# Performance work log

Measured on AMD Instinct MI355X. Metric: run time of the kernel, lower is better.

The kernel has to match this reference:

```python
import jax, jax.numpy as jnp
import numpy as np

HIDDEN = 1024
HEADS = 16
HEAD_DIM = HIDDEN // HEADS
LN_EPS = 1e-12


def _layer_norm(x, gamma, beta, eps=LN_EPS):
    mu = jnp.mean(x, axis=-1, keepdims=True)
    var = jnp.var(x, axis=-1, keepdims=True)
    return (x - mu) * jax.lax.rsqrt(var + eps) * gamma + beta


def setup_inputs() -> dict:
    key = jax.random.key(0)
    ks = jax.random.split(key, 8)
    B, S = 4, 2048
    hidden_states = jax.random.normal(ks[0], (B, S, HIDDEN), dtype=jnp.float32)
    attention_mask = jnp.zeros((B, 1, 1, S), dtype=jnp.float32)
    scale = 1.0 / np.sqrt(HIDDEN)
    return {
        "hidden_states": hidden_states,
        "attention_mask": attention_mask,
        "ln_gamma": jnp.ones((HIDDEN,), jnp.float32),
        "ln_beta": jnp.zeros((HIDDEN,), jnp.float32),
        "W_qkv": jax.random.normal(ks[1], (HIDDEN, 3 * HIDDEN), jnp.float32) * scale,
        "b_qkv": jnp.zeros((3 * HIDDEN,), jnp.float32),
        "W_out": jax.random.normal(ks[2], (HIDDEN, HIDDEN), jnp.float32) * scale,
        "b_out": jnp.zeros((HIDDEN,), jnp.float32),
    }


def reference(hidden_states, attention_mask, ln_gamma, ln_beta, W_qkv, b_qkv, W_out, b_out):
    B, S, H = hidden_states.shape
    x = _layer_norm(hidden_states, ln_gamma, ln_beta)
    qkv = x @ W_qkv + b_qkv  # [B, S, 3H]
    q, k, v = jnp.split(qkv, 3, axis=-1)
    q = q.reshape(B, S, HEADS, HEAD_DIM)
    k = k.reshape(B, S, HEADS, HEAD_DIM)
    v = v.reshape(B, S, HEADS, HEAD_DIM)
    # scores: [B, heads, q_len, kv_len]
    scores = jnp.einsum("bqhd,bkhd->bhqk", q, k) * (1.0 / np.sqrt(HEAD_DIM))
    scores = scores + attention_mask
    probs = jax.nn.softmax(scores, axis=-1)
    attn = jnp.einsum("bhqk,bkhd->bqhd", probs, v).reshape(B, S, H)
    out = attn @ W_out + b_out
    out = out + hidden_states  # residual (dropout is identity at p=0)
    return out
```

## Files before the change

kernel.cpp:

```cpp
#include <hip/hip_runtime.h>

#define SEQ 2048
#define HID 1024
#define NHEAD 16
#define HDIM 64
#define NB 4
#define NTOK (NB * SEQ)
#define NQKV (3 * HID)
#define LOG2E 1.44269504088896f
#define QSCALE (0.125f * LOG2E)

typedef __attribute__((ext_vector_type(8))) short bf16x8;
typedef __attribute__((ext_vector_type(4))) float f32x4;


__device__ __forceinline__ void glds16(const void* g, void* l) {
  __builtin_amdgcn_global_load_lds(
      (const __attribute__((address_space(1))) void*)g,
      (__attribute__((address_space(3))) void*)l, 16, 0, 0);
}

__device__ __forceinline__ ushort f2bf(float f) {
  union { float f; unsigned int u; } a; a.f = f;
  unsigned int u = a.u;
  return (ushort)((u + 0x7fffu + ((u >> 16) & 1u)) >> 16);
}

__device__ __forceinline__ unsigned int cvtpk(float a, float b) {
  unsigned int r;
  asm("v_cvt_pk_bf16_f32 %0, %1, %2" : "=v"(r) : "v"(a), "v"(b));
  return r;
}


__global__ __launch_bounds__(256) void ln_tr_fused(const float* __restrict__ x,
                                                   const float* __restrict__ g,
                                                   const float* __restrict__ be,
                                                   ushort* __restrict__ y,
                                                   const float* __restrict__ W0,
                                                   ushort* __restrict__ T0,
                                                   const float* __restrict__ W1,
                                                   ushort* __restrict__ T1) {
  __shared__ float t[32][33];
  const int tid = threadIdx.x;
  if (blockIdx.x < NTOK) {
    const int row = blockIdx.x;
    const float4 v = ((const float4*)(x + (size_t)row * HID))[tid];
    float s  = v.x + v.y + v.z + v.w;
    float sq = v.x * v.x + v.y * v.y + v.z * v.z + v.w * v.w;
    for (int o = 1; o < 64; o <<= 1) { s += __shfl_xor(s, o, 64); sq += __shfl_xor(sq, o, 64); }
    const int wv = tid >> 6;
    if ((tid & 63) == 0) { t[0][wv] = s; t[1][wv] = sq; }
    __syncthreads();
    s  = t[0][0] + t[0][1] + t[0][2] + t[0][3];
    sq = t[1][0] + t[1][1] + t[1][2] + t[1][3];
    const float mu  = s * (1.0f / HID);
    const float var = sq * (1.0f / HID) - mu * mu;
    const float rs  = rsqrtf(var + 1e-12f);
    const float4 gv = ((const float4*)g)[tid];
    const float4 bv = ((const float4*)be)[tid];
    ushort4 o;
    o.x = f2bf((v.x - mu) * rs * gv.x + bv.x);
    o.y = f2bf((v.y - mu) * rs * gv.y + bv.y);
    o.z = f2bf((v.z - mu) * rs * gv.z + bv.z);
    o.w = f2bf((v.w - mu) * rs * gv.w + bv.w);
    ((ushort4*)(y + (size_t)row * HID))[tid] = o;
    return;
  }
  const int bid = blockIdx.x - NTOK;
  const float* W; ushort* WT; int C, bx, by;
  if (bid < 3072) { W = W0; WT = T0; C = NQKV; bx = bid % 96; by = bid / 96; }
  else { const int b2 = bid - 3072; W = W1; WT = T1; C = HID; bx = b2 & 31; by = b2 >> 5; }
  const int R = HID;
  const int c0 = bx * 32, r0 = by * 32;
  const int tx = tid & 31, ty = tid >> 5;
  for (int j = 0; j < 4; ++j)
    t[ty + j * 8][tx] = W[(size_t)(r0 + ty + j * 8) * C + c0 + tx];
  __syncthreads();
  for (int j = 0; j < 4; ++j)
    WT[(size_t)(c0 + ty + j * 8) * R + r0 + tx] = f2bf(t[tx][ty + j * 8]);
}


__global__ __launch_bounds__(256) void v_transpose(const ushort* __restrict__ qkv,
                                                   ushort* __restrict__ vt) {
  __shared__ ushort t[64][66];
  const int s0 = blockIdx.x * 64, h = blockIdx.y, b = blockIdx.z;
  const size_t tokbase = (size_t)b * SEQ;
  for (int e = 0; e < 2; ++e) {
    const int c = e * 256 + threadIdx.x;
    const int sr = c >> 3, dc = c & 7;
    *(uint4*)&t[sr][dc * 8] =
        *(const uint4*)(qkv + (tokbase + s0 + sr) * NQKV + 2 * HID + h * HDIM + dc * 8);
  }
  __syncthreads();
  for (int e = 0; e < 2; ++e) {
    const int c = e * 256 + threadIdx.x;
    const int dr = c >> 3, sc = c & 7;
    ushort tmp[8];
    for (int j = 0; j < 8; ++j) tmp[j] = t[sc * 8 + j][dr];
    *(uint4*)(vt + ((size_t)(b * NHEAD + h) * HDIM + dr) * SEQ + s0 + sc * 8) = *(uint4*)tmp;
  }
}


template <int MODE>
__global__ __launch_bounds__(256) void gemm_bt(const ushort* __restrict__ A,
                                               const ushort* __restrict__ Bt,
                                               const float* __restrict__ bias,
                                               const float* __restrict__ resid,
                                               ushort* __restrict__ obf,
                                               float* __restrict__ of32,
                                               ushort* __restrict__ vtob,
                                               int M, int N, int K) {
  __shared__ ushort As[128 * 64];
  __shared__ ushort Bs[128 * 64];
  const int tid = threadIdx.x;
  const int lane = tid & 63, wv = tid >> 6;
  const int q = lane >> 4, li = lane & 15;
  const int nwgx = gridDim.x;
  const int hw = blockIdx.x + nwgx * blockIdx.y;
  const int cpx = (nwgx * gridDim.y) >> 3;
  const int logical = (hw & 7) * cpx + (hw >> 3);
  const int bx = logical % nwgx, by = logical / nwgx;
  const int m0 = by * 128, n0 = bx * 128;
  const int wm = (wv >> 1) * 64, wn = (wv & 1) * 64;
  f32x4 acc[4][4] = {};

  for (int kb = 0; kb < K; kb += 64) {
    for (int e = 0; e < 4; ++e) {
      const int chunk = (wv * 4 + e) * 64 + lane;
      const int row = chunk >> 3, slot = chunk & 7;
      const int kc = slot ^ (row & 7);
      glds16(A  + (size_t)(m0 + row) * K + kb + kc * 8, As + (wv * 4 + e) * 512);
      glds16(Bt + (size_t)(n0 + row) * K + kb + kc * 8, Bs + (wv * 4 + e) * 512);
    }
    __syncthreads();
    for (int ks = 0; ks < 2; ++ks) {
      const int kc = ks * 4 + q;
      bf16x8 af[4], bfr[4];
      for (int mi = 0; mi < 4; ++mi) {
        const int row = wm + mi * 16 + li;
        af[mi] = *(const bf16x8*)(As + (row * 8 + (kc ^ (row & 7))) * 8);
      }
      for (int ni = 0; ni < 4; ++ni) {
        const int row = wn + ni * 16 + li;
        bfr[ni] = *(const bf16x8*)(Bs + (row * 8 + (kc ^ (row & 7))) * 8);
      }
      for (int mi = 0; mi < 4; ++mi)
        for (int ni = 0; ni < 4; ++ni)
          acc[mi][ni] = __builtin_amdgcn_mfma_f32_16x16x32_bf16(af[mi], bfr[ni], acc[mi][ni], 0, 0, 0);
    }
    __syncthreads();
  }

  if (MODE == 0 && vtob != nullptr && n0 >= 2 * HID) {
    const int b = (m0 + wm) >> 11;
    const int sbase = (m0 + wm) & (SEQ - 1);
    for (int ni = 0; ni < 4; ++ni) {
      const int colv = n0 - 2 * HID + wn + ni * 16 + li;
      const int h = colv >> 6, d = colv & 63;
      const float bvs = bias[n0 + wn + ni * 16 + li];
      ushort* vbase = vtob + ((size_t)(b * NHEAD + h) * HDIM + d) * SEQ;
      for (int mi = 0; mi < 4; ++mi) {
        const int s = sbase + mi * 16 + q * 4;
        ushort4 o;
        o.x = f2bf(acc[mi][ni][0] + bvs);
        o.y = f2bf(acc[mi][ni][1] + bvs);
        o.z = f2bf(acc[mi][ni][2] + bvs);
        o.w = f2bf(acc[mi][ni][3] + bvs);
        *(ushort4*)(vbase + s) = o;
      }
    }
    return;
  }

  const float qs = (MODE == 0 && n0 < HID) ? QSCALE : 1.0f;
  for (int ni = 0; ni < 4; ++ni) {
    const int col = n0 + wn + ni * 16 + li;
    const float bvs = bias[col] * qs;
    for (int mi = 0; mi < 4; ++mi) {
      for (int r = 0; r < 4; ++r) {
        const int row = m0 + wm + mi * 16 + q * 4 + r;
        const float v = fmaf(acc[mi][ni][r], qs, bvs);
        if (MODE == 0) obf[(size_t)row * N + col] = f2bf(v);
        else           of32[(size_t)row * N + col] = v + resid[(size_t)row * N + col];
      }
    }
  }
}


__global__ __launch_bounds__(512) void flash_attn(const ushort* __restrict__ qkv,
                                                  const ushort* __restrict__ vt,
                                                  const float* __restrict__ mask,
                                                  ushort* __restrict__ outa) {
  __shared__ ushort KV[2][8192];
  const int tid = threadIdx.x, lane = tid & 63, wv = tid >> 6;
  const int quad = lane >> 4, li = lane & 15;
  const int wq = wv * 32;
  constexpr int NT = SEQ / 64;

  const int L = blockIdx.x + 8 * blockIdx.y + 128 * blockIdx.z;
  const int xcd = L & 7, rrem = L >> 3;
  const int p = (rrem >> 3) * 8 + xcd;
  const int qt0 = rrem & 7, h = p & 15, b = p >> 4;

  const size_t tokbase = (size_t)b * SEQ;
  const size_t vtbase = (size_t)(b * NHEAD + h) * HDIM * SEQ;
  const float* mrow = mask + (size_t)b * SEQ;

  for (int e = 0; e < 4; ++e) {
    const int c = (wv * 4 + e) * 64 + lane;
    const int row = c >> 3, slot = c & 7;
    const int kc = slot ^ (row & 7);
    const int gtok = qt0 * 128 + (row & 127) + (row >> 7) * 1024;
    glds16(qkv + (tokbase + gtok) * NQKV + h * HDIM + kc * 8,
           &KV[0][0] + (wv * 4 + e) * 512);
  }
  __syncthreads();

  bf16x8 qf[2][2];
  for (int ks = 0; ks < 2; ++ks) {
    const int kc = ks * 4 + quad;
    for (int nq = 0; nq < 2; ++nq) {
      const int row = wq + nq * 16 + li;
      qf[ks][nq] = *(const bf16x8*)(&KV[0][0] + (row * 8 + (kc ^ (row & 7))) * 8);
    }
  }
  __syncthreads();

  int koff[2][4], voff[2][4];
  for (int ks = 0; ks < 2; ++ks) {
    const int kc = ks * 4 + quad;
    for (int i = 0; i < 4; ++i) {
      const int row = i * 16 + li;
      koff[ks][i] = (row * 8 + (kc ^ (row & 7))) * 8;
      voff[ks][i] = koff[ks][i] + 4096;
    }
  }
  unsigned ksoff, vsoff;
  {
    const int c = wv * 64 + lane;
    const int row = c >> 3, slot = c & 7;
    const int kc = slot ^ (row & 7);
    const int gkv = (row & 0x23) | ((row & 0x0c) << 1) | ((row & 0x10) >> 2);
    ksoff = (unsigned)((tokbase + gkv) * NQKV + HID + h * HDIM + kc * 8);
    vsoff = (unsigned)(vtbase + (size_t)row * SEQ + kc * 8);
  }

  const unsigned int one2 = 0x3F803F80u;
  bf16x8 ones;
  for (int j = 0; j < 4; ++j) ((unsigned int*)&ones)[j] = one2;

  f32x4 accO[2][4] = {};
  f32x4 accL[2] = {};

  auto stage_kv = [&](int t, int buf) {
    const unsigned ka = (unsigned)(t * (64 * NQKV));
    const unsigned va = (unsigned)(t * 64);
    glds16(qkv + ksoff + ka, &KV[buf][0] + wv * 512);
    glds16(vt + vsoff + va,  &KV[buf][4096] + wv * 512);
  };

  auto mask_fetch = [&](int t, f32x4 (&mk)[4]) {
    const int kv0 = (t & (NT - 1)) * 64;
    for (int m = 0; m < 4; ++m) {
      const float4 v = *(const float4*)(mrow + kv0 + (m >> 1) * 32 + quad * 8 + (m & 1) * 4);
      mk[m][0] = v.x * LOG2E; mk[m][1] = v.y * LOG2E;
      mk[m][2] = v.z * LOG2E; mk[m][3] = v.w * LOG2E;
    }
  };

  auto compute = [&](int t, int buf, f32x4 (&mkc)[4], f32x4 (&mkn)[4]) {
    mask_fetch(t + 1, mkn);

    const ushort* Kb = &KV[buf][0];

    f32x4 sc[2][4];
    __builtin_amdgcn_s_setprio(1);
    for (int ks = 0; ks < 2; ++ks) {
      bf16x8 kf[4];
      for (int m = 0; m < 4; ++m)
        kf[m] = *(const bf16x8*)(Kb + koff[ks][m]);
      for (int nq = 0; nq < 2; ++nq)
        for (int m = 0; m < 4; ++m)
          sc[nq][m] = __builtin_amdgcn_mfma_f32_16x16x32_bf16(
              kf[m], qf[ks][nq], ks == 0 ? mkc[m] : sc[nq][m], 0, 0, 0);
    }
    __builtin_amdgcn_s_setprio(0);

    for (int ks = 0; ks < 2; ++ks) {
      bf16x8 vf[4];
      for (int nd = 0; nd < 4; ++nd)
        vf[nd] = *(const bf16x8*)(Kb + voff[ks][nd]);
      unsigned int pk[2][2][2];
      for (int nq = 0; nq < 2; ++nq)
        for (int mm = 0; mm < 2; ++mm) {
          const int m = 2 * ks + mm;
          const float p0 = __builtin_amdgcn_exp2f(sc[nq][m][0]);
          const float p1 = __builtin_amdgcn_exp2f(sc[nq][m][1]);
          const float p2 = __builtin_amdgcn_exp2f(sc[nq][m][2]);
          const float p3 = __builtin_amdgcn_exp2f(sc[nq][m][3]);
          pk[nq][mm][0] = cvtpk(p0, p1);
          pk[nq][mm][1] = cvtpk(p2, p3);
        }
      __builtin_amdgcn_s_setprio(1);
      for (int mq = 0; mq < 2; ++mq) {
        bf16x8 pf;
        ((unsigned int*)&pf)[0] = pk[mq][0][0];
        ((unsigned int*)&pf)[1] = pk[mq][0][1];
        ((unsigned int*)&pf)[2] = pk[mq][1][0];
        ((unsigned int*)&pf)[3] = pk[mq][1][1];
        for (int nd = 0; nd < 4; ++nd)
          accO[mq][nd] = __builtin_amdgcn_mfma_f32_16x16x32_bf16(pf, vf[nd], accO[mq][nd], 0, 0, 0);
        accL[mq] = __builtin_amdgcn_mfma_f32_16x16x32_bf16(pf, ones, accL[mq], 0, 0, 0);
      }
      __builtin_amdgcn_s_setprio(0);
    }
  };

  f32x4 mkA[4], mkB[4];
  mask_fetch(0, mkA);
  stage_kv(0, 0);
  for (int t = 0; t < NT; t += 2) {
    __syncthreads();
    stage_kv(t + 1, 1);
    compute(t, 0, mkA, mkB);
    __syncthreads();
    if (t + 2 < SEQ / 64) stage_kv(t + 2, 0);
    compute(t + 1, 1, mkB, mkA);
  }

  for (int mq = 0; mq < 2; ++mq)
    for (int r = 0; r < 4; ++r) {
      const float inv = 1.0f / accL[mq][r];
      const size_t tok = tokbase + qt0 * 128 + ((size_t)(wv >> 2) << 10) +
                         (wv & 3) * 32 + mq * 16 + quad * 4 + r;
      for (int nd = 0; nd < 4; ++nd)
        outa[tok * HID + h * HDIM + nd * 16 + li] = f2bf(accO[mq][nd][r] * inv);
    }
}


extern "C" void kernel_launch(void* const* d_in, const int* in_sizes, int n_in,
                              void* d_out, int out_size, void* d_ws, size_t ws_size,
                              hipStream_t stream) {
  const float* hidden = (const float*)d_in[0];
  const float* mask   = (const float*)d_in[1];
  const float* gamma  = (const float*)d_in[2];
  const float* beta   = (const float*)d_in[3];
  const float* Wqkv   = (const float*)d_in[4];
  const float* bqkv   = (const float*)d_in[5];
  const float* Wout   = (const float*)d_in[6];
  const float* bout   = (const float*)d_in[7];
  float* out = (float*)d_out;

  char* ws = (char*)d_ws;
  const bool fuse_vt = ws_size >= ((size_t)104 << 20);
  ushort* x_bf  = (ushort*)(ws);
  ushort* wqkvT = (ushort*)(ws + ((size_t)16 << 20));
  ushort* woutT = (ushort*)(ws + ((size_t)22 << 20));
  ushort* qkvb  = (ushort*)(ws + ((size_t)24 << 20));
  ushort* attnb = (ushort*)(ws + ((size_t)72 << 20));
  ushort* vtb   = fuse_vt ? (ushort*)(ws + ((size_t)88 << 20))
                          : (ushort*)(ws);

  ln_tr_fused<<<NTOK + 4096, 256, 0, stream>>>(hidden, gamma, beta, x_bf,
                                               Wqkv, wqkvT, Wout, woutT);
  gemm_bt<0><<<dim3(NQKV / 128, NTOK / 128), 256, 0, stream>>>(
      x_bf, wqkvT, bqkv, nullptr, qkvb, nullptr, fuse_vt ? vtb : nullptr, NTOK, NQKV, HID);
  if (!fuse_vt)
    v_transpose<<<dim3(SEQ / 64, NHEAD, NB), 256, 0, stream>>>(qkvb, vtb);
  flash_attn<<<dim3(SEQ / 256, NHEAD, NB), 512, 0, stream>>>(qkvb, vtb, mask, attnb);
  gemm_bt<1><<<dim3(HID / 128, NTOK / 128), 256, 0, stream>>>(
      attnb, woutT, bout, hidden, nullptr, out, nullptr, NTOK, HID, HID);
}
```

Before: 284.3 us.

## Process KV tiles in pairs per stage to halve barriers in flash attention

The attention loop now stages two 64-token KV tiles per buffer, doubling shared memory per block to 64 KB, and computes both QK^T score sets before running softmax and PV on each. This halves the number of __syncthreads and staging rounds and gives more independent MFMA work between barriers for latency hiding. In exchange, register pressure rises from holding two score tiles live, and the larger LDS footprint may reduce occupancy.

```diff
diff --git a/kernel.cpp b/kernel.cpp
--- a/kernel.cpp
+++ b/kernel.cpp
@@ -195,16 +195,16 @@
                                                   const ushort* __restrict__ vt,
                                                   const float* __restrict__ mask,
                                                   ushort* __restrict__ outa) {
-  __shared__ ushort KV[2][8192];
+  __shared__ ushort KV[2][16384];
   const int tid = threadIdx.x, lane = tid & 63, wv = tid >> 6;
   const int quad = lane >> 4, li = lane & 15;
   const int wq = wv * 32;
-  constexpr int NT = SEQ / 64;
+  constexpr int NP = SEQ / 128;
 
   const int L = blockIdx.x + 8 * blockIdx.y + 128 * blockIdx.z;
   const int xcd = L & 7, rrem = L >> 3;
-  const int p = (rrem >> 3) * 8 + xcd;
-  const int qt0 = rrem & 7, h = p & 15, b = p >> 4;
+  const int pg = (rrem >> 3) * 8 + xcd;
+  const int qt0 = rrem & 7, h = pg & 15, b = pg >> 4;
 
   const size_t tokbase = (size_t)b * SEQ;
   const size_t vtbase = (size_t)(b * NHEAD + h) * HDIM * SEQ;
@@ -256,15 +256,16 @@
   f32x4 accO[2][4] = {};
   f32x4 accL[2] = {};
 
-  auto stage_kv = [&](int t, int buf) {
-    const unsigned ka = (unsigned)(t * (64 * NQKV));
-    const unsigned va = (unsigned)(t * 64);
-    glds16(qkv + ksoff + ka, &KV[buf][0] + wv * 512);
-    glds16(vt + vsoff + va,  &KV[buf][4096] + wv * 512);
-  };
-
-  auto mask_fetch = [&](int t, f32x4 (&mk)[4]) {
-    const int kv0 = (t & (NT - 1)) * 64;
+  auto stage_pair = [&](int p, int buf) {
+    const unsigned ka = (unsigned)(p * (128 * NQKV));
+    const unsigned va = (unsigned)(p * 128);
+    glds16(qkv + ksoff + ka,              &KV[buf][0]     + wv * 512);
+    glds16(qkv + ksoff + ka + 64 * NQKV,  &KV[buf][8192]  + wv * 512);
+    glds16(vt  + vsoff + va,              &KV[buf][4096]  + wv * 512);
+    glds16(vt  + vsoff + va + 64,         &KV[buf][12288] + wv * 512);
+  };
+
+  auto mfetch = [&](int kv0, f32x4 (&mk)[4]) {
     for (int m = 0; m < 4; ++m) {
       const float4 v = *(const float4*)(mrow + kv0 + (m >> 1) * 32 + quad * 8 + (m & 1) * 4);
       mk[m][0] = v.x * LOG2E; mk[m][1] = v.y * LOG2E;
@@ -272,12 +273,7 @@
     }
   };
 
-  auto compute = [&](int t, int buf, f32x4 (&mkc)[4], f32x4 (&mkn)[4]) {
-    mask_fetch(t + 1, mkn);
-
-    const ushort* Kb = &KV[buf][0];
-
-    f32x4 sc[2][4];
+  auto qk = [&](const ushort* Kb, f32x4 (&mk)[4], f32x4 (&sc)[2][4]) {
     __builtin_amdgcn_s_setprio(1);
     for (int ks = 0; ks < 2; ++ks) {
       bf16x8 kf[4];
@@ -286,10 +282,12 @@
       for (int nq = 0; nq < 2; ++nq)
         for (int m = 0; m < 4; ++m)
           sc[nq][m] = __builtin_amdgcn_mfma_f32_16x16x32_bf16(
-              kf[m], qf[ks][nq], ks == 0 ? mkc[m] : sc[nq][m], 0, 0, 0);
+              kf[m], qf[ks][nq], ks == 0 ? mk[m] : sc[nq][m], 0, 0, 0);
     }
     __builtin_amdgcn_s_setprio(0);
-
+  };
+
+  auto smpv = [&](const ushort* Kb, f32x4 (&sc)[2][4]) {
     for (int ks = 0; ks < 2; ++ks) {
       bf16x8 vf[4];
       for (int nd = 0; nd < 4; ++nd)
@@ -320,16 +318,29 @@
     }
   };
 
+  auto compute = [&](int p, int buf, f32x4 (&mkc)[4], f32x4 (&mkn)[4]) {
+    const ushort* B0 = &KV[buf][0];
+    const ushort* B1 = &KV[buf][8192];
+    f32x4 mk1[4];
+    mfetch(p * 128 + 64, mk1);
+    f32x4 sc0[2][4], sc1[2][4];
+    qk(B0, mkc, sc0);
+    qk(B1, mk1, sc1);
+    mfetch(((p + 1) & (NP - 1)) * 128, mkn);
+    smpv(B0, sc0);
+    smpv(B1, sc1);
+  };
+
   f32x4 mkA[4], mkB[4];
-  mask_fetch(0, mkA);
-  stage_kv(0, 0);
-  for (int t = 0; t < NT; t += 2) {
-    __syncthreads();
-    stage_kv(t + 1, 1);
-    compute(t, 0, mkA, mkB);
-    __syncthreads();
-    if (t + 2 < SEQ / 64) stage_kv(t + 2, 0);
-    compute(t + 1, 1, mkB, mkA);
+  mfetch(0, mkA);
+  stage_pair(0, 0);
+  for (int p = 0; p < NP; p += 2) {
+    __syncthreads();
+    stage_pair(p + 1, 1);
+    compute(p, 0, mkA, mkB);
+    __syncthreads();
+    if (p + 2 < NP) stage_pair(p + 2, 0);
+    compute(p + 1, 1, mkB, mkA);
   }
 
   for (int mq = 0; mq < 2; ++mq)
```

Measured after the change: 285.1 us. About the same (+0.3%).
